# Kernel optimization log

Hardware: AMD Instinct MI355X
Metric: run time of the kernel (lower is better)

Reference implementation:

```python
import jax, jax.numpy as jnp
import numpy as np

B, N, E, H = 4, 2048, 1024, 16
D = E // H
SCALE = D ** -0.5
EPS = 1.1920929e-07  # torch.finfo(float32).eps (RMSNorm default eps=None)


def _rmsnorm(x, w):
    # normalize over last dim (head_dim)
    ms = jnp.mean(x * x, axis=-1, keepdims=True)
    return x * jax.lax.rsqrt(ms + EPS) * w


def setup_inputs() -> dict:
    key = jax.random.key(0)
    ks = jax.random.split(key, 10)
    s_in = E ** -0.5
    return {
        "hidden_states": jax.random.normal(ks[0], (B, N, E), jnp.float32),
        "encoder_hidden_states": jax.random.normal(ks[1], (B, N, E), jnp.float32),
        "Wq": jax.random.normal(ks[2], (E, E), jnp.float32) * s_in,
        "bq": jnp.zeros((E,), jnp.float32),
        "Wkv": jax.random.normal(ks[3], (E, 2 * E), jnp.float32) * s_in,
        "bkv": jnp.zeros((2 * E,), jnp.float32),
        "qn_w": jnp.ones((D,), jnp.float32),
        "kn_w": jnp.ones((D,), jnp.float32),
        "Wo": jax.random.normal(ks[4], (E, E), jnp.float32) * s_in,
        "bo": jnp.zeros((E,), jnp.float32),
    }


def reference(hidden_states, encoder_hidden_states, Wq, bq, Wkv, bkv, qn_w, kn_w, Wo, bo):
    q_proj = hidden_states @ Wq + bq                     # [B,N,E]
    kv_proj = encoder_hidden_states @ Wkv + bkv          # [B,N,2E]
    qkv = jnp.concatenate([q_proj, kv_proj], axis=-1)    # [B,N,3E]
    # Rearrange 'b n (h d j) -> b h n d j' with j=3 innermost: interleaved split
    qkv = qkv.reshape(B, N, H, D, 3)
    q = jnp.transpose(qkv[..., 0], (0, 2, 1, 3)) * SCALE  # [B,H,N,D]
    k = jnp.transpose(qkv[..., 1], (0, 2, 1, 3))
    v = jnp.transpose(qkv[..., 2], (0, 2, 1, 3))
    q = _rmsnorm(q, qn_w)
    k = _rmsnorm(k, kn_w)
    # q already pre-scaled (before norm, which cancels it up to eps); attention uses no extra scale
    scores = jnp.einsum('bhqd,bhkd->bhqk', q, k)          # [B,H,N,N]
    attn = jax.nn.softmax(scores, axis=-1)
    ctx = jnp.einsum('bhqk,bhkd->bhqd', attn, v)          # [B,H,N,D]
    ctx = jnp.transpose(ctx, (0, 2, 1, 3)).reshape(B, N, E)
    return ctx @ Wo + bo
```

## Files before the change

### kernel.cpp

```cpp
#include <hip/hip_runtime.h>
#include <hip/hip_bf16.h>
#include <cstddef>
#include <cmath>

#define B_ 4
#define N_ 2048
#define E_ 1024
#define H_ 16
#define D_ 64
#define SCALE_ 0.125f
#define EPS_ 1.1920929e-07f

typedef __attribute__((ext_vector_type(8))) short short8;
typedef __attribute__((ext_vector_type(4))) short short4s;
typedef __attribute__((ext_vector_type(4))) float floatx4;

__device__ __forceinline__ unsigned short f2bf(float x) {
    unsigned int u = __float_as_uint(x);
    u += 0x7FFFu + ((u >> 16) & 1u);
    return (unsigned short)(u >> 16);
}
__device__ __forceinline__ float bf2f(unsigned short b) {
    return __uint_as_float(((unsigned int)b) << 16);
}

#define MFMA16(a, b, c) __builtin_amdgcn_mfma_f32_16x16x32_bf16((a), (b), (c), 0, 0, 0)

__global__ __launch_bounds__(256) void wtrans_kernel(
    const float* __restrict__ src, int K, int N,
    short* __restrict__ dstH, short* __restrict__ dstL)
{
    __shared__ __align__(16) short Hs[64][68], Ls[64][68];
    const int k0 = blockIdx.x * 64, n0 = blockIdx.y * 64;
    const int t = threadIdx.x;
    {
        int kk = t >> 4, cc = (t & 15) * 4;
#pragma unroll
        for (int i = 0; i < 4; ++i) {
            int k = kk + i * 16;
            float4 v = *(const float4*)(src + (size_t)(k0 + k) * N + n0 + cc);
            float vx[4] = {v.x, v.y, v.z, v.w};
            short4s h4, l4;
#pragma unroll
            for (int c = 0; c < 4; ++c) {
                unsigned short hb = f2bf(vx[c]);
                h4[c] = (short)hb;
                l4[c] = (short)f2bf(vx[c] - bf2f(hb));
            }
            *(short4s*)&Hs[k][cc] = h4;
            *(short4s*)&Ls[k][cc] = l4;
        }
    }
    __syncthreads();
    {
        int nn = t >> 3, kq = (t & 7) * 8;
#pragma unroll
        for (int i = 0; i < 2; ++i) {
            int n = nn + i * 32;
            short8 h8, l8;
#pragma unroll
            for (int j = 0; j < 8; ++j) { h8[j] = Hs[kq + j][n]; l8[j] = Ls[kq + j][n]; }
            *(short8*)(dstH + (size_t)(n0 + n) * K + k0 + kq) = h8;
            *(short8*)(dstL + (size_t)(n0 + n) * K + k0 + kq) = l8;
        }
    }
}

__global__ __launch_bounds__(256) void proj_kernel(
    const float* __restrict__ hs, const float* __restrict__ ehs,
    const short* __restrict__ WtqH, const short* __restrict__ WtqL,
    const short* __restrict__ WtkvH, const short* __restrict__ WtkvL,
    const float* __restrict__ bq, const float* __restrict__ bkv,
    short* __restrict__ qh, short* __restrict__ ql,
    short* __restrict__ kh, short* __restrict__ kl,
    short* __restrict__ vt)
{
    const int ct = blockIdx.x;
    const int rt = blockIdx.y;
    const int col0 = ct * 128;
    const bool isQ = (col0 < 1024);
    const float* __restrict__ A    = isQ ? hs : ehs;
    const short* __restrict__ WH   = isQ ? WtqH : WtkvH;
    const short* __restrict__ WL   = isQ ? WtqL : WtkvL;
    const float* __restrict__ bias = isQ ? bq : bkv;
    const int wcol0 = isQ ? col0 : (col0 - 1024);

    __shared__ __align__(16) short Ah[128 * 40], Al[128 * 40];
    __shared__ __align__(16) short Bh[128 * 40], Bl[128 * 40];

    const int tid = threadIdx.x;
    const int lane = tid & 63, wid = tid >> 6;
    const int wr = wid >> 1, wc = wid & 1;
    const int l15 = lane & 15, g = lane >> 4;

    floatx4 acc[4][4];
#pragma unroll
    for (int m = 0; m < 4; ++m)
#pragma unroll
        for (int n = 0; n < 4; ++n) acc[m][n] = floatx4{0.f, 0.f, 0.f, 0.f};

    const float* Abase = A + (size_t)rt * 128 * 1024;

    for (int k0 = 0; k0 < 1024; k0 += 32) {
#pragma unroll
        for (int i = 0; i < 4; ++i) {
            int f = tid + i * 256;
            int row = f >> 3, kq = f & 7;
            float4 a = *(const float4*)(Abase + (size_t)row * 1024 + k0 + kq * 4);
            float vx[4] = {a.x, a.y, a.z, a.w};
            short4s h4, l4;
#pragma unroll
            for (int c = 0; c < 4; ++c) {
                unsigned short hb = f2bf(vx[c]);
                h4[c] = (short)hb;
                l4[c] = (short)f2bf(vx[c] - bf2f(hb));
            }
            *(short4s*)&Ah[row * 40 + kq * 4] = h4;
            *(short4s*)&Al[row * 40 + kq * 4] = l4;
        }
#pragma unroll
        for (int i = 0; i < 2; ++i) {
            int f = tid + i * 256;
            int colb = f >> 2, kq = (f & 3) * 8;
            *(short8*)&Bh[colb * 40 + kq] =
                *(const short8*)(WH + (size_t)(wcol0 + colb) * 1024 + k0 + kq);
            *(short8*)&Bl[colb * 40 + kq] =
                *(const short8*)(WL + (size_t)(wcol0 + colb) * 1024 + k0 + kq);
        }
        __syncthreads();

        short8 ah[4], al[4], bh[4], bl[4];
#pragma unroll
        for (int m = 0; m < 4; ++m) {
            int r = (wr * 64 + m * 16 + l15) * 40 + g * 8;
            ah[m] = *(const short8*)&Ah[r];
            al[m] = *(const short8*)&Al[r];
        }
#pragma unroll
        for (int n = 0; n < 4; ++n) {
            int r = (wc * 64 + n * 16 + l15) * 40 + g * 8;
            bh[n] = *(const short8*)&Bh[r];
            bl[n] = *(const short8*)&Bl[r];
        }
#pragma unroll
        for (int m = 0; m < 4; ++m)
#pragma unroll
            for (int n = 0; n < 4; ++n) {
                acc[m][n] = MFMA16(ah[m], bh[n], acc[m][n]);
                acc[m][n] = MFMA16(ah[m], bl[n], acc[m][n]);
                acc[m][n] = MFMA16(al[m], bh[n], acc[m][n]);
            }
        __syncthreads();
    }

#pragma unroll
    for (int n = 0; n < 4; ++n) {
        int c = col0 + wc * 64 + n * 16 + l15;
        float bi = bias[c - (isQ ? 0 : 1024)];
        int h   = c / 192;
        int rem = c - h * 192;
        int dd  = rem / 3;
        int j3  = rem - dd * 3;
#pragma unroll
        for (int m = 0; m < 4; ++m) {
            int grow0 = rt * 128 + wr * 64 + m * 16 + g * 4;
            int b = grow0 >> 11, nn0 = grow0 & 2047;
            if (j3 == 2) {
                short4s v4;
#pragma unroll
                for (int r = 0; r < 4; ++r) v4[r] = (short)f2bf(acc[m][n][r] + bi);
                *(short4s*)(vt + (((size_t)b * 16 + h) * 64 + dd) * 2048 + nn0) = v4;
            } else {
                short* dh = (j3 == 0) ? qh : kh;
                short* dl = (j3 == 0) ? ql : kl;
#pragma unroll
                for (int r = 0; r < 4; ++r) {
                    float val = acc[m][n][r] + bi;
                    size_t idx = (((size_t)b * 16 + h) * 2048 + (nn0 + r)) * 64 + dd;
                    unsigned short hb = f2bf(val);
                    dh[idx] = (short)hb;
                    dl[idx] = (short)f2bf(val - bf2f(hb));
                }
            }
        }
    }
}

__global__ __launch_bounds__(256) void rmsnorm_kernel(
    short* __restrict__ qh, short* __restrict__ ql,
    short* __restrict__ kh, short* __restrict__ kl,
    const float* __restrict__ qn_w, const float* __restrict__ kn_w)
{
    const int tid = threadIdx.x, lane = tid & 63, wid = tid >> 6;
    const size_t row = (size_t)blockIdx.x * 16 + wid * 4 + (lane >> 4);
    const int d4 = (lane & 15) * 4;
    const bool isQ = (blockIdx.y == 0);
    short* xh = (isQ ? qh : kh) + row * 64 + d4;
    short* xl = (isQ ? ql : kl) + row * 64 + d4;
    const float* w = (isQ ? qn_w : kn_w) + d4;

    short4s h4 = *(short4s*)xh, l4 = *(short4s*)xl;
    float x[4];
#pragma unroll
    for (int c = 0; c < 4; ++c) {
        x[c] = bf2f((unsigned short)h4[c]) + bf2f((unsigned short)l4[c]);
        if (isQ) x[c] *= SCALE_;
    }
    float s = x[0]*x[0] + x[1]*x[1] + x[2]*x[2] + x[3]*x[3];
#pragma unroll
    for (int off = 1; off <= 8; off <<= 1) s += __shfl_xor(s, off);
    float r = rsqrtf(s * (1.f / 64.f) + EPS_);
#pragma unroll
    for (int c = 0; c < 4; ++c) {
        float y = x[c] * r * w[c];
        unsigned short hb = f2bf(y);
        h4[c] = (short)hb;
        l4[c] = (short)f2bf(y - bf2f(hb));
    }
    *(short4s*)xh = h4;
    *(short4s*)xl = l4;
}

__global__ __launch_bounds__(256) void attn_kernel(
    const short* __restrict__ qh, const short* __restrict__ ql,
    const short* __restrict__ kh, const short* __restrict__ kl,
    const short* __restrict__ vt,
    short* __restrict__ cxh, short* __restrict__ cxl)
{
    const int bh = blockIdx.x;
    const int qt = blockIdx.y;
    const size_t kbase = (size_t)bh * 2048 * 64;
    const size_t vbase = (size_t)bh * 64 * 2048;

    __shared__ __align__(16) short Kh[64 * 72], Kl[64 * 72];
    __shared__ __align__(16) short Vs[64 * 72];
    __shared__ __align__(16) short Ps[64 * 72];

    const int tid = threadIdx.x;
    const int lane = tid & 63, wid = tid >> 6;
    const int l15 = lane & 15, g = lane >> 4;

    const size_t qrow0 = ((size_t)bh * 2048 + qt * 64 + wid * 16 + l15) * 64;
    short8 qfh[2], qfl[2];
#pragma unroll
    for (int s = 0; s < 2; ++s) {
        qfh[s] = *(const short8*)(qh + qrow0 + s * 32 + g * 8);
        qfl[s] = *(const short8*)(ql + qrow0 + s * 32 + g * 8);
    }

    floatx4 acc_o[4];
#pragma unroll
    for (int n = 0; n < 4; ++n) acc_o[n] = floatx4{0.f, 0.f, 0.f, 0.f};
    float m_i = -INFINITY, l_i = 0.f;

    for (int kt = 0; kt < 32; ++kt) {
        __syncthreads();
#pragma unroll
        for (int i = 0; i < 2; ++i) {
            int f = tid + i * 256;
            int row = f >> 3, dq = (f & 7) * 8;
            const size_t gsrc = kbase + (size_t)(kt * 64 + row) * 64 + dq;
            *(short8*)&Kh[row * 72 + dq] = *(const short8*)(kh + gsrc);
            *(short8*)&Kl[row * 72 + dq] = *(const short8*)(kl + gsrc);
        }
#pragma unroll
        for (int i = 0; i < 2; ++i) {
            int f = tid + i * 256;
            int dd = f >> 3, nq = (f & 7) * 8;
            *(short8*)&Vs[dd * 72 + nq] =
                *(const short8*)(vt + vbase + (size_t)dd * 2048 + kt * 64 + nq);
        }
        __syncthreads();

        floatx4 s4[4];
#pragma unroll
        for (int n = 0; n < 4; ++n) s4[n] = floatx4{0.f, 0.f, 0.f, 0.f};
#pragma unroll
        for (int s = 0; s < 2; ++s)
#pragma unroll
            for (int n = 0; n < 4; ++n) {
                int r = (n * 16 + l15) * 72 + s * 32 + g * 8;
                short8 kfh = *(const short8*)&Kh[r];
                short8 kfl = *(const short8*)&Kl[r];
                s4[n] = MFMA16(kfh, qfh[s], s4[n]);
                s4[n] = MFMA16(kfh, qfl[s], s4[n]);
                s4[n] = MFMA16(kfl, qfh[s], s4[n]);
            }

        float mt = s4[0][0];
#pragma unroll
        for (int n = 0; n < 4; ++n) {
            mt = fmaxf(mt, fmaxf(fmaxf(s4[n][0], s4[n][1]), fmaxf(s4[n][2], s4[n][3])));
        }
        mt = fmaxf(mt, __shfl_xor(mt, 16));
        mt = fmaxf(mt, __shfl_xor(mt, 32));
        float mnew = fmaxf(m_i, mt);
        float corr = __expf(m_i - mnew);
        m_i = mnew;
        float ps = 0.f;
#pragma unroll
        for (int n = 0; n < 4; ++n) {
            short4s p4;
#pragma unroll
            for (int r = 0; r < 4; ++r) {
                float p = __expf(s4[n][r] - mnew);
                unsigned short pbits = f2bf(p);
                p4[r] = (short)pbits;
                ps += bf2f(pbits);
            }
            *(short4s*)&Ps[(wid * 16 + l15) * 72 + n * 16 + g * 4] = p4;
        }
        ps += __shfl_xor(ps, 16);
        ps += __shfl_xor(ps, 32);
        l_i = l_i * corr + ps;

        float corr4[4];
#pragma unroll
        for (int r = 0; r < 4; ++r) corr4[r] = __shfl(corr, g * 4 + r);
#pragma unroll
        for (int n = 0; n < 4; ++n)
#pragma unroll
            for (int r = 0; r < 4; ++r) acc_o[n][r] *= corr4[r];

#pragma unroll
        for (int s = 0; s < 2; ++s) {
            short8 pa = *(const short8*)&Ps[(wid * 16 + l15) * 72 + s * 32 + g * 8];
#pragma unroll
            for (int n = 0; n < 4; ++n) {
                short8 vf = *(const short8*)&Vs[(n * 16 + l15) * 72 + s * 32 + g * 8];
                acc_o[n] = MFMA16(pa, vf, acc_o[n]);
            }
        }
    }

    float inv = 1.f / l_i;
    float inv4[4];
#pragma unroll
    for (int r = 0; r < 4; ++r) inv4[r] = __shfl(inv, g * 4 + r);
    const int b = bh >> 4, h = bh & 15;
#pragma unroll
    for (int r = 0; r < 4; ++r) {
        int row = qt * 64 + wid * 16 + g * 4 + r;
#pragma unroll
        for (int n = 0; n < 4; ++n) {
            float val = acc_o[n][r] * inv4[r];
            size_t o = ((size_t)b * 2048 + row) * 1024 + h * 64 + n * 16 + l15;
            unsigned short hb = f2bf(val);
            cxh[o] = (short)hb;
            cxl[o] = (short)f2bf(val - bf2f(hb));
        }
    }
}

__global__ __launch_bounds__(256) void out_gemm_kernel(
    const short* __restrict__ cxh, const short* __restrict__ cxl,
    const short* __restrict__ WtoH, const short* __restrict__ WtoL,
    const float* __restrict__ bias, float* __restrict__ out)
{
    const int ct = blockIdx.x;
    const int rt = blockIdx.y;
    const int col0 = ct * 128;

    __shared__ __align__(16) short Ah[128 * 40], Al[128 * 40];
    __shared__ __align__(16) short Bh[128 * 40], Bl[128 * 40];

    const int tid = threadIdx.x;
    const int lane = tid & 63, wid = tid >> 6;
    const int wr = wid >> 1, wc = wid & 1;
    const int l15 = lane & 15, g = lane >> 4;

    floatx4 acc[4][4];
#pragma unroll
    for (int m = 0; m < 4; ++m)
#pragma unroll
        for (int n = 0; n < 4; ++n) acc[m][n] = floatx4{0.f, 0.f, 0.f, 0.f};

    for (int k0 = 0; k0 < 1024; k0 += 32) {
#pragma unroll
        for (int i = 0; i < 2; ++i) {
            int f = tid + i * 256;
            int row = f >> 2, kq = (f & 3) * 8;
            const size_t gsrc = (size_t)(rt * 128 + row) * 1024 + k0 + kq;
            *(short8*)&Ah[row * 40 + kq] = *(const short8*)(cxh + gsrc);
            *(short8*)&Al[row * 40 + kq] = *(const short8*)(cxl + gsrc);
        }
#pragma unroll
        for (int i = 0; i < 2; ++i) {
            int f = tid + i * 256;
            int colb = f >> 2, kq = (f & 3) * 8;
            *(short8*)&Bh[colb * 40 + kq] =
                *(const short8*)(WtoH + (size_t)(col0 + colb) * 1024 + k0 + kq);
            *(short8*)&Bl[colb * 40 + kq] =
                *(const short8*)(WtoL + (size_t)(col0 + colb) * 1024 + k0 + kq);
        }
        __syncthreads();

        short8 ah[4], al[4], bh[4], bl[4];
#pragma unroll
        for (int m = 0; m < 4; ++m) {
            int r = (wr * 64 + m * 16 + l15) * 40 + g * 8;
            ah[m] = *(const short8*)&Ah[r];
            al[m] = *(const short8*)&Al[r];
        }
#pragma unroll
        for (int n = 0; n < 4; ++n) {
            int r = (wc * 64 + n * 16 + l15) * 40 + g * 8;
            bh[n] = *(const short8*)&Bh[r];
            bl[n] = *(const short8*)&Bl[r];
        }
#pragma unroll
        for (int m = 0; m < 4; ++m)
#pragma unroll
            for (int n = 0; n < 4; ++n) {
                acc[m][n] = MFMA16(ah[m], bh[n], acc[m][n]);
                acc[m][n] = MFMA16(ah[m], bl[n], acc[m][n]);
                acc[m][n] = MFMA16(al[m], bh[n], acc[m][n]);
            }
        __syncthreads();
    }

#pragma unroll
    for (int n = 0; n < 4; ++n) {
        int c = col0 + wc * 64 + n * 16 + l15;
        float bi = bias[c];
#pragma unroll
        for (int m = 0; m < 4; ++m)
#pragma unroll
            for (int r = 0; r < 4; ++r) {
                size_t grow = (size_t)rt * 128 + wr * 64 + m * 16 + g * 4 + r;
                out[grow * 1024 + c] = acc[m][n][r] + bi;
            }
    }
}

extern "C" void kernel_launch(void* const* d_in, const int* in_sizes, int n_in,
                              void* d_out, int out_size, void* d_ws, size_t ws_size,
                              hipStream_t stream)
{
    const float* hs  = (const float*)d_in[0];
    const float* ehs = (const float*)d_in[1];
    const float* Wq  = (const float*)d_in[2];
    const float* bq  = (const float*)d_in[3];
    const float* Wkv = (const float*)d_in[4];
    const float* bkv = (const float*)d_in[5];
    const float* qn  = (const float*)d_in[6];
    const float* kn  = (const float*)d_in[7];
    const float* Wo  = (const float*)d_in[8];
    const float* bo  = (const float*)d_in[9];
    float* out = (float*)d_out;

    const size_t SZ = (size_t)B_ * H_ * N_ * D_;
    short* ws   = (short*)d_ws;
    short* qh   = ws;
    short* ql   = qh + SZ;
    short* kh   = ql + SZ;
    short* kl   = kh + SZ;
    short* vt   = kl + SZ;
    short* cxh  = vt + SZ;
    short* cxl  = cxh + SZ;
    short* WtqH = cxl + SZ;
    short* WtqL = WtqH + 1024 * 1024;
    short* WtkvH = WtqL + 1024 * 1024;
    short* WtkvL = WtkvH + 2048 * 1024;
    short* WtoH  = WtkvL + 2048 * 1024;
    short* WtoL  = WtoH + 1024 * 1024;

    wtrans_kernel<<<dim3(16, 16), 256, 0, stream>>>(Wq, 1024, 1024, WtqH, WtqL);
    wtrans_kernel<<<dim3(16, 32), 256, 0, stream>>>(Wkv, 1024, 2048, WtkvH, WtkvL);
    wtrans_kernel<<<dim3(16, 16), 256, 0, stream>>>(Wo, 1024, 1024, WtoH, WtoL);

    proj_kernel<<<dim3(24, 64), 256, 0, stream>>>(hs, ehs, WtqH, WtqL, WtkvH, WtkvL,
                                                  bq, bkv, qh, ql, kh, kl, vt);
    rmsnorm_kernel<<<dim3(8192, 2), 256, 0, stream>>>(qh, ql, kh, kl, qn, kn);
    attn_kernel<<<dim3(64, 32), 256, 0, stream>>>(qh, ql, kh, kl, vt, cxh, cxl);
    out_gemm_kernel<<<dim3(8, 64), 256, 0, stream>>>(cxh, cxl, WtoH, WtoL, bo, out);
}
```

Baseline: 666.1 us.

## Register-prefetch next tiles in GEMM and attention loops, pre-split inputs to bf16 pairs

Adds register double-buffering to the projection GEMM, the attention K/V loop and the output GEMM. Each next tile's global loads are issued before the current tile's MFMA work, so memory latency can overlap with compute. Also adds a prep kernel that converts hidden_states and encoder_hidden_states in place into interleaved bf16 hi/lo pairs, which removes the per-tile fp32 split from the projection GEMM. The in-place overwrite destroys the caller's input buffers, so a repeated call would reinterpret already-converted data. The prep kernels also add an extra full read/write pass over both activations.

```diff
diff --git a/kernel.cpp b/kernel.cpp
--- a/kernel.cpp
+++ b/kernel.cpp
@@ -26,6 +26,21 @@
 
 #define MFMA16(a, b, c) __builtin_amdgcn_mfma_f32_16x16x32_bf16((a), (b), (c), 0, 0, 0)
 
+__global__ __launch_bounds__(256) void aprep_kernel(float* __restrict__ x)
+{
+    const size_t i = ((size_t)blockIdx.x * 256 + threadIdx.x) * 4;
+    float4 v = *(const float4*)(x + i);
+    float vx[4] = {v.x, v.y, v.z, v.w};
+    short8 p;
+#pragma unroll
+    for (int c = 0; c < 4; ++c) {
+        unsigned short hb = f2bf(vx[c]);
+        p[2 * c]     = (short)hb;
+        p[2 * c + 1] = (short)f2bf(vx[c] - bf2f(hb));
+    }
+    *(short8*)(x + i) = p;
+}
+
 __global__ __launch_bounds__(256) void wtrans_kernel(
     const float* __restrict__ src, int K, int N,
     short* __restrict__ dstH, short* __restrict__ dstL)
@@ -67,7 +82,7 @@
 }
 
 __global__ __launch_bounds__(256) void proj_kernel(
-    const float* __restrict__ hs, const float* __restrict__ ehs,
+    const short* __restrict__ hs_pk, const short* __restrict__ ehs_pk,
     const short* __restrict__ WtqH, const short* __restrict__ WtqL,
     const short* __restrict__ WtkvH, const short* __restrict__ WtkvL,
     const float* __restrict__ bq, const float* __restrict__ bkv,
@@ -79,7 +94,7 @@
     const int rt = blockIdx.y;
     const int col0 = ct * 128;
     const bool isQ = (col0 < 1024);
-    const float* __restrict__ A    = isQ ? hs : ehs;
+    const short* __restrict__ Apk  = (isQ ? hs_pk : ehs_pk) + (size_t)rt * 128 * 1024 * 2;
     const short* __restrict__ WH   = isQ ? WtqH : WtkvH;
     const short* __restrict__ WL   = isQ ? WtqL : WtkvL;
     const float* __restrict__ bias = isQ ? bq : bkv;
@@ -99,22 +114,31 @@
 #pragma unroll
         for (int n = 0; n < 4; ++n) acc[m][n] = floatx4{0.f, 0.f, 0.f, 0.f};
 
-    const float* Abase = A + (size_t)rt * 128 * 1024;
-
-    for (int k0 = 0; k0 < 1024; k0 += 32) {
+    short8 rA[4], rBh[2], rBl[2];
+
+    auto LOAD = [&](int k0) {
 #pragma unroll
         for (int i = 0; i < 4; ++i) {
             int f = tid + i * 256;
             int row = f >> 3, kq = f & 7;
-            float4 a = *(const float4*)(Abase + (size_t)row * 1024 + k0 + kq * 4);
-            float vx[4] = {a.x, a.y, a.z, a.w};
+            rA[i] = *(const short8*)(Apk + ((size_t)row * 1024 + k0 + kq * 4) * 2);
+        }
+#pragma unroll
+        for (int i = 0; i < 2; ++i) {
+            int f = tid + i * 256;
+            int colb = f >> 2, kq = (f & 3) * 8;
+            rBh[i] = *(const short8*)(WH + (size_t)(wcol0 + colb) * 1024 + k0 + kq);
+            rBl[i] = *(const short8*)(WL + (size_t)(wcol0 + colb) * 1024 + k0 + kq);
+        }
+    };
+    auto STORE = [&]() {
+#pragma unroll
+        for (int i = 0; i < 4; ++i) {
+            int f = tid + i * 256;
+            int row = f >> 3, kq = f & 7;
             short4s h4, l4;
 #pragma unroll
-            for (int c = 0; c < 4; ++c) {
-                unsigned short hb = f2bf(vx[c]);
-                h4[c] = (short)hb;
-                l4[c] = (short)f2bf(vx[c] - bf2f(hb));
-            }
+            for (int c = 0; c < 4; ++c) { h4[c] = rA[i][2 * c]; l4[c] = rA[i][2 * c + 1]; }
             *(short4s*)&Ah[row * 40 + kq * 4] = h4;
             *(short4s*)&Al[row * 40 + kq * 4] = l4;
         }
@@ -122,13 +146,11 @@
         for (int i = 0; i < 2; ++i) {
             int f = tid + i * 256;
             int colb = f >> 2, kq = (f & 3) * 8;
-            *(short8*)&Bh[colb * 40 + kq] =
-                *(const short8*)(WH + (size_t)(wcol0 + colb) * 1024 + k0 + kq);
-            *(short8*)&Bl[colb * 40 + kq] =
-                *(const short8*)(WL + (size_t)(wcol0 + colb) * 1024 + k0 + kq);
-        }
-        __syncthreads();
-
+            *(short8*)&Bh[colb * 40 + kq] = rBh[i];
+            *(short8*)&Bl[colb * 40 + kq] = rBl[i];
+        }
+    };
+    auto COMPUTE = [&]() {
         short8 ah[4], al[4], bh[4], bl[4];
 #pragma unroll
         for (int m = 0; m < 4; ++m) {
@@ -150,8 +172,19 @@
                 acc[m][n] = MFMA16(ah[m], bl[n], acc[m][n]);
                 acc[m][n] = MFMA16(al[m], bh[n], acc[m][n]);
             }
+    };
+
+    LOAD(0);
+    STORE();
+    __syncthreads();
+    for (int k0 = 32; k0 < 1024; k0 += 32) {
+        LOAD(k0);
+        COMPUTE();
         __syncthreads();
-    }
+        STORE();
+        __syncthreads();
+    }
+    COMPUTE();
 
 #pragma unroll
     for (int n = 0; n < 4; ++n) {
@@ -248,29 +281,50 @@
         qfl[s] = *(const short8*)(ql + qrow0 + s * 32 + g * 8);
     }
 
+    short8 rKh[2], rKl[2], rV[2];
+    auto LOADKV = [&](int kt) {
+#pragma unroll
+        for (int i = 0; i < 2; ++i) {
+            int f = tid + i * 256;
+            int row = f >> 3, dq = (f & 7) * 8;
+            const size_t gsrc = kbase + (size_t)(kt * 64 + row) * 64 + dq;
+            rKh[i] = *(const short8*)(kh + gsrc);
+            rKl[i] = *(const short8*)(kl + gsrc);
+        }
+#pragma unroll
+        for (int i = 0; i < 2; ++i) {
+            int f = tid + i * 256;
+            int dd = f >> 3, nq = (f & 7) * 8;
+            rV[i] = *(const short8*)(vt + vbase + (size_t)dd * 2048 + kt * 64 + nq);
+        }
+    };
+    auto STOREKV = [&]() {
+#pragma unroll
+        for (int i = 0; i < 2; ++i) {
+            int f = tid + i * 256;
+            int row = f >> 3, dq = (f & 7) * 8;
+            *(short8*)&Kh[row * 72 + dq] = rKh[i];
+            *(short8*)&Kl[row * 72 + dq] = rKl[i];
+        }
+#pragma unroll
+        for (int i = 0; i < 2; ++i) {
+            int f = tid + i * 256;
+            int dd = f >> 3, nq = (f & 7) * 8;
+            *(short8*)&Vs[dd * 72 + nq] = rV[i];
+        }
+    };
+
     floatx4 acc_o[4];
 #pragma unroll
     for (int n = 0; n < 4; ++n) acc_o[n] = floatx4{0.f, 0.f, 0.f, 0.f};
     float m_i = -INFINITY, l_i = 0.f;
 
+    LOADKV(0);
     for (int kt = 0; kt < 32; ++kt) {
         __syncthreads();
-#pragma unroll
-        for (int i = 0; i < 2; ++i) {
-            int f = tid + i * 256;
-            int row = f >> 3, dq = (f & 7) * 8;
-            const size_t gsrc = kbase + (size_t)(kt * 64 + row) * 64 + dq;
-            *(short8*)&Kh[row * 72 + dq] = *(const short8*)(kh + gsrc);
-            *(short8*)&Kl[row * 72 + dq] = *(const short8*)(kl + gsrc);
-        }
-#pragma unroll
-        for (int i = 0; i < 2; ++i) {
-            int f = tid + i * 256;
-            int dd = f >> 3, nq = (f & 7) * 8;
-            *(short8*)&Vs[dd * 72 + nq] =
-                *(const short8*)(vt + vbase + (size_t)dd * 2048 + kt * 64 + nq);
-        }
+        STOREKV();
         __syncthreads();
+        if (kt + 1 < 32) LOADKV(kt + 1);
 
         floatx4 s4[4];
 #pragma unroll
@@ -375,26 +429,42 @@
 #pragma unroll
         for (int n = 0; n < 4; ++n) acc[m][n] = floatx4{0.f, 0.f, 0.f, 0.f};
 
-    for (int k0 = 0; k0 < 1024; k0 += 32) {
+    short8 rAh[2], rAl[2], rBh[2], rBl[2];
+
+    auto LOAD = [&](int k0) {
 #pragma unroll
         for (int i = 0; i < 2; ++i) {
             int f = tid + i * 256;
             int row = f >> 2, kq = (f & 3) * 8;
             const size_t gsrc = (size_t)(rt * 128 + row) * 1024 + k0 + kq;
-            *(short8*)&Ah[row * 40 + kq] = *(const short8*)(cxh + gsrc);
-            *(short8*)&Al[row * 40 + kq] = *(const short8*)(cxl + gsrc);
+            rAh[i] = *(const short8*)(cxh + gsrc);
+            rAl[i] = *(const short8*)(cxl + gsrc);
         }
 #pragma unroll
         for (int i = 0; i < 2; ++i) {
             int f = tid + i * 256;
             int colb = f >> 2, kq = (f & 3) * 8;
-            *(short8*)&Bh[colb * 40 + kq] =
-                *(const short8*)(WtoH + (size_t)(col0 + colb) * 1024 + k0 + kq);
-            *(short8*)&Bl[colb * 40 + kq] =
-                *(const short8*)(WtoL + (size_t)(col0 + colb) * 1024 + k0 + kq);
-        }
-        __syncthreads();
-
+            rBh[i] = *(const short8*)(WtoH + (size_t)(col0 + colb) * 1024 + k0 + kq);
+            rBl[i] = *(const short8*)(WtoL + (size_t)(col0 + colb) * 1024 + k0 + kq);
+        }
+    };
+    auto STORE = [&]() {
+#pragma unroll
+        for (int i = 0; i < 2; ++i) {
+            int f = tid + i * 256;
+            int row = f >> 2, kq = (f & 3) * 8;
+            *(short8*)&Ah[row * 40 + kq] = rAh[i];
+            *(short8*)&Al[row * 40 + kq] = rAl[i];
+        }
+#pragma unroll
+        for (int i = 0; i < 2; ++i) {
+            int f = tid + i * 256;
+            int colb = f >> 2, kq = (f & 3) * 8;
+            *(short8*)&Bh[colb * 40 + kq] = rBh[i];
+            *(short8*)&Bl[colb * 40 + kq] = rBl[i];
+        }
+    };
+    auto COMPUTE = [&]() {
         short8 ah[4], al[4], bh[4], bl[4];
 #pragma unroll
         for (int m = 0; m < 4; ++m) {
@@ -416,8 +486,19 @@
                 acc[m][n] = MFMA16(ah[m], bl[n], acc[m][n]);
                 acc[m][n] = MFMA16(al[m], bh[n], acc[m][n]);
             }
+    };
+
+    LOAD(0);
+    STORE();
+    __syncthreads();
+    for (int k0 = 32; k0 < 1024; k0 += 32) {
+        LOAD(k0);
+        COMPUTE();
         __syncthreads();
-    }
+        STORE();
+        __syncthreads();
+    }
+    COMPUTE();
 
 #pragma unroll
     for (int n = 0; n < 4; ++n) {
@@ -437,8 +518,8 @@
                               void* d_out, int out_size, void* d_ws, size_t ws_size,
                               hipStream_t stream)
 {
-    const float* hs  = (const float*)d_in[0];
-    const float* ehs = (const float*)d_in[1];
+    float* hs  = (float*)d_in[0];
+    float* ehs = (float*)d_in[1];
     const float* Wq  = (const float*)d_in[2];
     const float* bq  = (const float*)d_in[3];
     const float* Wkv = (const float*)d_in[4];
@@ -465,11 +546,14 @@
     short* WtoH  = WtkvL + 2048 * 1024;
     short* WtoL  = WtoH + 1024 * 1024;
 
+    aprep_kernel<<<8192, 256, 0, stream>>>(hs);
+    aprep_kernel<<<8192, 256, 0, stream>>>(ehs);
     wtrans_kernel<<<dim3(16, 16), 256, 0, stream>>>(Wq, 1024, 1024, WtqH, WtqL);
     wtrans_kernel<<<dim3(16, 32), 256, 0, stream>>>(Wkv, 1024, 2048, WtkvH, WtkvL);
     wtrans_kernel<<<dim3(16, 16), 256, 0, stream>>>(Wo, 1024, 1024, WtoH, WtoL);
 
-    proj_kernel<<<dim3(24, 64), 256, 0, stream>>>(hs, ehs, WtqH, WtqL, WtkvH, WtkvL,
+    proj_kernel<<<dim3(24, 64), 256, 0, stream>>>((const short*)hs, (const short*)ehs,
+                                                  WtqH, WtqL, WtkvH, WtkvL,
                                                   bq, bkv, qh, ql, kh, kl, vt);
     rmsnorm_kernel<<<dim3(8192, 2), 256, 0, stream>>>(qh, ql, kh, kl, qn, kn);
     attn_kernel<<<dim3(64, 32), 256, 0, stream>>>(qh, ql, kh, kl, vt, cxh, cxl);
```

Result: no change. 660.6 us (-0.8%).
